# Kernel optimization log

Measured on AMD Instinct MI355X. Metric: run time of the kernel, lower is better.

Reference implementation:

```python
import jax, jax.numpy as jnp
import numpy as np

B, LQ, LK, H, NH = 2, 2048, 2048, 1024, 16
HD = H // NH


def setup_inputs() -> dict:
    key = jax.random.key(0)
    ks = jax.random.split(key, 7)
    s = 1.0 / np.sqrt(H)
    return {
        "decoder_hidden": jax.random.normal(ks[0], (B, LQ, H), jnp.float32),
        "encoder_hidden": jax.random.normal(ks[1], (B, LK, H), jnp.float32),
        "encoder_attention_mask": jnp.ones((B, LK), jnp.int32),
        "Wq": jax.random.normal(ks[2], (H, H), jnp.float32) * s,
        "Wk": jax.random.normal(ks[3], (H, H), jnp.float32) * s,
        "Wv": jax.random.normal(ks[4], (H, H), jnp.float32) * s,
        "Wo": jax.random.normal(ks[5], (H, H), jnp.float32) * s,
        "bo": jnp.zeros((H,), jnp.float32),
    }


def reference(decoder_hidden, encoder_hidden, encoder_attention_mask, Wq, Wk, Wv, Wo, bo):
    # nn.Linear(bias=False): y = x @ W.T
    Q = jnp.einsum('bqh,oh->bqo', decoder_hidden, Wq)
    K = jnp.einsum('bkh,oh->bko', encoder_hidden, Wk)
    V = jnp.einsum('bkh,oh->bko', encoder_hidden, Wv)
    # [B, NH, L, HD]
    Q = Q.reshape(B, LQ, NH, HD).transpose(0, 2, 1, 3)
    K = K.reshape(B, LK, NH, HD).transpose(0, 2, 1, 3)
    V = V.reshape(B, LK, NH, HD).transpose(0, 2, 1, 3)
    scale = jnp.float32(HD) ** -0.5
    scores = jnp.einsum('bhqd,bhkd->bhqk', Q, K) * scale
    mask = (encoder_attention_mask[:, None, None, :] != 0)  # [B,1,1,LK]
    scores = jnp.where(mask, scores, -jnp.inf)
    weights = jax.nn.softmax(scores, axis=-1)
    # dropout is identity in eval mode
    context = jnp.einsum('bhqk,bhkd->bhqd', weights, V)
    context = context.transpose(0, 2, 1, 3).reshape(B, LQ, H)
    output = jnp.einsum('bqh,oh->bqo', context, Wo) + bo
    return output, weights
```

## Files before the change

### kernel.cpp

```cpp
#include <hip/hip_runtime.h>
#include <hip/hip_bf16.h>
#include <stdint.h>

typedef __attribute__((ext_vector_type(8))) short short8;
typedef __attribute__((ext_vector_type(4))) short s16x4;
typedef __attribute__((ext_vector_type(4))) float f32x4;

#define MFMA16(a,b,c)    __builtin_amdgcn_mfma_f32_16x16x32_bf16(a,b,c,0,0,0)
#define MFMA16K16(a,b,c) __builtin_amdgcn_mfma_f32_16x16x16bf16_1k(a,b,c,0,0,0)

static __device__ inline void gload_lds16(const void* g, void* l) {
  __builtin_amdgcn_global_load_lds((const __attribute__((address_space(1))) uint32_t*)g,
                                   (__attribute__((address_space(3))) uint32_t*)l, 16, 0, 0);
}

__global__ __launch_bounds__(256) void cvt_all(
    const float* __restrict__ dh, const float* __restrict__ eh,
    const float* __restrict__ Wq, const float* __restrict__ Wk,
    const float* __restrict__ Wv, const float* __restrict__ Wo,
    __hip_bfloat16* __restrict__ dhb, __hip_bfloat16* __restrict__ ehb,
    __hip_bfloat16* __restrict__ wqb, __hip_bfloat16* __restrict__ wkb,
    __hip_bfloat16* __restrict__ wvb, __hip_bfloat16* __restrict__ wob)
{
  int idx = blockIdx.x * 256 + threadIdx.x;
  const float* src; __hip_bfloat16* dst; int off;
  if      (idx <  524288) { src=dh; dst=dhb; off=idx; }
  else if (idx < 1048576) { src=eh; dst=ehb; off=idx-524288; }
  else if (idx < 1179648) { src=Wq; dst=wqb; off=idx-1048576; }
  else if (idx < 1310720) { src=Wk; dst=wkb; off=idx-1179648; }
  else if (idx < 1441792) { src=Wv; dst=wvb; off=idx-1310720; }
  else                    { src=Wo; dst=wob; off=idx-1441792; }
  float4 a = ((const float4*)src)[off*2+0];
  float4 b = ((const float4*)src)[off*2+1];
  union { short8 v; __hip_bfloat16 h[8]; } u;
  u.h[0]=__float2bfloat16(a.x); u.h[1]=__float2bfloat16(a.y);
  u.h[2]=__float2bfloat16(a.z); u.h[3]=__float2bfloat16(a.w);
  u.h[4]=__float2bfloat16(b.x); u.h[5]=__float2bfloat16(b.y);
  u.h[6]=__float2bfloat16(b.z); u.h[7]=__float2bfloat16(b.w);
  ((short8*)dst)[off] = u.v;
}

__device__ inline void gemm_core(const __hip_bfloat16* __restrict__ A,
                                 const __hip_bfloat16* __restrict__ W,
                                 int bm, int bn, int K, f32x4 (&acc)[4][4]) {
  __shared__ __hip_bfloat16 sA[128*64];
  __shared__ __hip_bfloat16 sB[128*64];
  const int t = threadIdx.x, lane = t & 63, wvi = t >> 6, g = lane >> 4, i = lane & 15;
  const int wm = wvi >> 1, wn = wvi & 1;
  const f32x4 z4 = {0.f,0.f,0.f,0.f};
  for (int m=0;m<4;m++) for (int n=0;n<4;n++) acc[m][n]=z4;
  const int nkt = K >> 6;
  for (int kt=0; kt<nkt; ++kt) {
    for (int c=0;c<4;c++) {
      int idx = c*256+t, row = idx>>3, slot = idx&7;
      int sc = (slot ^ (row&7))*8;
      gload_lds16(A + (size_t)(bm*128+row)*K + kt*64 + sc, (char*)sA + c*4096 + wvi*1024);
    }
    for (int c=0;c<4;c++) {
      int idx = c*256+t, row = idx>>3, slot = idx&7;
      int sc = (slot ^ (row&7))*8;
      gload_lds16(W + (size_t)(bn*128+row)*K + kt*64 + sc, (char*)sB + c*4096 + wvi*1024);
    }
    __syncthreads();
    short8 af[4][2], bf[4][2];
    for (int m=0;m<4;m++) {
      int row = wm*64 + m*16 + i;
      af[m][0] = *(const short8*)&sA[row*64 + ((g     ^ (row&7)))*8];
      af[m][1] = *(const short8*)&sA[row*64 + (((4+g) ^ (row&7)))*8];
    }
    for (int n=0;n<4;n++) {
      int row = wn*64 + n*16 + i;
      bf[n][0] = *(const short8*)&sB[row*64 + ((g     ^ (row&7)))*8];
      bf[n][1] = *(const short8*)&sB[row*64 + (((4+g) ^ (row&7)))*8];
    }
    for (int m=0;m<4;m++) for (int n=0;n<4;n++) {
      acc[m][n] = MFMA16(af[m][0], bf[n][0], acc[m][n]);
      acc[m][n] = MFMA16(af[m][1], bf[n][1], acc[m][n]);
    }
    __syncthreads();
  }
}

__global__ __launch_bounds__(256) void gemm_qkv(
    const __hip_bfloat16* __restrict__ dhb, const __hip_bfloat16* __restrict__ ehb,
    const __hip_bfloat16* __restrict__ wqp, const __hip_bfloat16* __restrict__ wkp,
    const __hip_bfloat16* __restrict__ wvp,
    __hip_bfloat16* __restrict__ Qb, __hip_bfloat16* __restrict__ Kb,
    __hip_bfloat16* __restrict__ Vt) {
  const int zz = blockIdx.z;
  const __hip_bfloat16* A = (zz==0) ? dhb : ehb;
  const __hip_bfloat16* W = (zz==0) ? wqp : (zz==1 ? wkp : wvp);
  f32x4 acc[4][4];
  gemm_core(A, W, blockIdx.x, blockIdx.y, 1024, acc);
  const int t = threadIdx.x, lane=t&63, w_=t>>6, g=lane>>4, i=lane&15;
  const int wm=w_>>1, wn=w_&1;
  if (zz != 2) {
    __hip_bfloat16* C = (zz==0) ? Qb : Kb;
    for (int m=0;m<4;m++) for (int n=0;n<4;n++) for (int r=0;r<4;r++) {
      int row = blockIdx.x*128 + wm*64 + m*16 + 4*g + r;
      int col = blockIdx.y*128 + wn*64 + n*16 + i;
      C[(size_t)row*1024 + col] = __float2bfloat16(acc[m][n][r]);
    }
  } else {
    for (int m=0;m<4;m++) for (int n=0;n<4;n++) {
      int row0 = blockIdx.x*128 + wm*64 + m*16 + 4*g;
      int bb = row0 >> 11, kin = row0 & 2047;
      int o = blockIdx.y*128 + wn*64 + n*16 + i;
      int hh = o >> 6, dd = o & 63;
      union { s16x4 v; __hip_bfloat16 h4[4]; } u;
      for (int r=0;r<4;r++) u.h4[r] = __float2bfloat16(acc[m][n][r]);
      *(s16x4*)&Vt[((size_t)((bb*16+hh)*64+dd))*2048 + kin] = u.v;
    }
  }
}

__global__ __launch_bounds__(256) void gemm_out(
    const __hip_bfloat16* __restrict__ ctx, const __hip_bfloat16* __restrict__ wop,
    const float* __restrict__ bias, float* __restrict__ out) {
  f32x4 acc[4][4];
  gemm_core(ctx, wop, blockIdx.x, blockIdx.y, 1024, acc);
  const int t = threadIdx.x, lane=t&63, w_=t>>6, g=lane>>4, i=lane&15;
  const int wm=w_>>1, wn=w_&1;
  for (int m=0;m<4;m++) for (int n=0;n<4;n++) for (int r=0;r<4;r++) {
    int row = blockIdx.x*128 + wm*64 + m*16 + 4*g + r;
    int col = blockIdx.y*128 + wn*64 + n*16 + i;
    out[(size_t)row*1024 + col] = acc[m][n][r] + bias[col];
  }
}

__global__ __launch_bounds__(256, 4) void attn_kernel(
    const __hip_bfloat16* __restrict__ Qb, const __hip_bfloat16* __restrict__ Kb,
    const __hip_bfloat16* __restrict__ Vt, const int* __restrict__ mask,
    float* __restrict__ wout, __hip_bfloat16* __restrict__ ctx)
{
  __shared__ char smem[32768];
  const int t = threadIdx.x, lane = t&63, wv_ = t>>6, g = lane>>4, i = lane&15;
  const int qt = blockIdx.x, bh = blockIdx.y, b = bh>>4, h = bh&15;
  const int q0 = qt*64 + wv_*16;
  const float scale = 0.125f;
  const f32x4 z4 = {0.f,0.f,0.f,0.f};

  short8 qf[2];
  { const __hip_bfloat16* qrow = Qb + (size_t)(b*2048 + q0 + i)*1024 + h*64;
    qf[0] = *(const short8*)(qrow + g*8);
    qf[1] = *(const short8*)(qrow + 32 + g*8); }

  f32x4 acc[4];
  for (int z=0;z<4;z++) acc[z] = z4;
  float lsum = 0.0f;

  const int* mbase = mask + b*2048;

#define STAGE_KV(buf, kt_) do { \
    _Pragma("unroll") \
    for (int c=0;c<2;c++) { \
      int idx_ = c*256 + t; int row_ = idx_>>3, slot_ = idx_&7; \
      int sc_ = (slot_ ^ (row_&7)) * 8; \
      gload_lds16(Kb + (size_t)(b*2048 + (kt_)*64 + row_)*1024 + h*64 + sc_, \
                  smem + (buf)*8192 + c*4096 + wv_*1024); \
      gload_lds16(Vt + (size_t)((b*16+h)*64 + row_)*2048 + (kt_)*64 + sc_, \
                  smem + 16384 + (buf)*8192 + c*4096 + wv_*1024); \
    } } while(0)

#define STAGE_K(buf, kt_) do { \
    _Pragma("unroll") \
    for (int c=0;c<2;c++) { \
      int idx_ = c*256 + t; int row_ = idx_>>3, slot_ = idx_&7; \
      int sc_ = (slot_ ^ (row_&7)) * 8; \
      gload_lds16(Kb + (size_t)(b*2048 + (kt_)*64 + row_)*1024 + h*64 + sc_, \
                  smem + (buf)*8192 + c*4096 + wv_*1024); \
    } } while(0)

  int cur = 0;
  STAGE_KV(0, 0);
  __syncthreads();
  for (int kt=0; kt<32; ++kt) {
    if (kt+1 < 32) STAGE_KV(cur^1, kt+1);
    const __hip_bfloat16* sKc = (const __hip_bfloat16*)(smem + cur*8192);
    const __hip_bfloat16* sVc = (const __hip_bfloat16*)(smem + 16384 + cur*8192);
    #pragma unroll
    for (int cb=0; cb<4; ++cb) {
      int row = cb*16 + i;
      short8 kf0 = *(const short8*)&sKc[row*64 + ((g     ^ (row&7)))*8];
      short8 kf1 = *(const short8*)&sKc[row*64 + (((4+g) ^ (row&7)))*8];
      f32x4 st = MFMA16(kf0, qf[0], z4);
      st = MFMA16(kf1, qf[1], st);
      int4 m4 = *(const int4*)&mbase[kt*64 + cb*16 + 4*g];
      float p0 = m4.x ? __expf(st[0]*scale) : 0.0f;
      float p1 = m4.y ? __expf(st[1]*scale) : 0.0f;
      float p2 = m4.z ? __expf(st[2]*scale) : 0.0f;
      float p3 = m4.w ? __expf(st[3]*scale) : 0.0f;
      lsum += (p0+p1)+(p2+p3);
      union { s16x4 v; __hip_bfloat16 hh[4]; } pk;
      pk.hh[0] = __float2bfloat16(p0);
      pk.hh[1] = __float2bfloat16(p1);
      pk.hh[2] = __float2bfloat16(p2);
      pk.hh[3] = __float2bfloat16(p3);
      #pragma unroll
      for (int blk=0; blk<4; ++blk) {
        int vrow = blk*16 + i;
        const s16x4 vtf = *(const s16x4*)&sVc[vrow*64 +
            (((2*cb + (g>>1)) ^ (vrow&7)))*8 + 4*(g&1)];
        acc[blk] = MFMA16K16(pk.v, vtf, acc[blk]);
      }
    }
    __syncthreads();
    cur ^= 1;
  }

  lsum += __shfl_xor(lsum, 16);
  lsum += __shfl_xor(lsum, 32);
  const float linvq = 1.0f / lsum;

  float linvr[4];
  #pragma unroll
  for (int r=0;r<4;r++) linvr[r] = __shfl(linvq, (lane & 48) | (4*g + r));

  #pragma unroll
  for (int blk=0;blk<4;blk++)
    #pragma unroll
    for (int r=0;r<4;r++) {
      int q = q0 + 4*g + r;
      ctx[(size_t)(b*2048 + q)*1024 + h*64 + blk*16 + i] =
          __float2bfloat16(acc[blk][r]*linvr[r]);
    }

  STAGE_K(0, 0);
  __syncthreads();

  char* sT = smem + 16384 + wv_*4096;

  cur = 0;
  for (int kt=0; kt<32; ++kt) {
    if (kt+1 < 32) STAGE_K(cur^1, kt+1);
    asm volatile("" ::: "memory");
    const __hip_bfloat16* sKc = (const __hip_bfloat16*)(smem + cur*8192);
    #pragma unroll
    for (int cb=0; cb<4; ++cb) {
      int row = cb*16 + i;
      short8 kf0 = *(const short8*)&sKc[row*64 + ((g     ^ (row&7)))*8];
      short8 kf1 = *(const short8*)&sKc[row*64 + (((4+g) ^ (row&7)))*8];
      f32x4 st = MFMA16(kf0, qf[0], z4);
      st = MFMA16(kf1, qf[1], st);
      int4 m4 = *(const int4*)&mbase[kt*64 + cb*16 + 4*g];
      f32x4 w4;
      w4[0] = m4.x ? __expf(st[0]*scale)*linvq : 0.f;
      w4[1] = m4.y ? __expf(st[1]*scale)*linvq : 0.f;
      w4[2] = m4.z ? __expf(st[2]*scale)*linvq : 0.f;
      w4[3] = m4.w ? __expf(st[3]*scale)*linvq : 0.f;
      *(f32x4*)(sT + i*256 + (((cb*4 + g) ^ i) * 16)) = w4;
    }
    #pragma unroll
    for (int s=0; s<4; ++s) {
      int rho = 4*s + g;
      f32x4 w4 = *(const f32x4*)(sT + rho*256 + ((i ^ rho) * 16));
      __builtin_nontemporal_store(w4,
          (f32x4*)&wout[((size_t)bh*2048 + q0 + rho)*2048 + kt*64 + i*4]);
    }
    asm volatile("s_waitcnt vmcnt(4)" ::: "memory");
    __builtin_amdgcn_s_barrier();
    cur ^= 1;
  }
#undef STAGE_KV
#undef STAGE_K
}

extern "C" void kernel_launch(void* const* d_in, const int* in_sizes, int n_in,
                              void* d_out, int out_size, void* d_ws, size_t ws_size,
                              hipStream_t stream) {
  const float* dh  = (const float*)d_in[0];
  const float* eh  = (const float*)d_in[1];
  const int*  mask = (const int*)d_in[2];
  const float* Wq  = (const float*)d_in[3];
  const float* Wk  = (const float*)d_in[4];
  const float* Wv  = (const float*)d_in[5];
  const float* Wo  = (const float*)d_in[6];
  const float* bo  = (const float*)d_in[7];
  float* out  = (float*)d_out;
  float* wout = out + (size_t)2*2048*1024;

  char* ws = (char*)d_ws;
  __hip_bfloat16* dhb = (__hip_bfloat16*)(ws + 0);
  __hip_bfloat16* ehb = (__hip_bfloat16*)(ws + 8388608);
  __hip_bfloat16* wqb = (__hip_bfloat16*)(ws + 16777216);
  __hip_bfloat16* wkb = (__hip_bfloat16*)(ws + 18874368);
  __hip_bfloat16* wvb = (__hip_bfloat16*)(ws + 20971520);
  __hip_bfloat16* wob = (__hip_bfloat16*)(ws + 23068672);
  __hip_bfloat16* Qb  = (__hip_bfloat16*)(ws + 25165824);
  __hip_bfloat16* Kb  = (__hip_bfloat16*)(ws + 33554432);
  __hip_bfloat16* Vtb = (__hip_bfloat16*)(ws + 41943040);
  __hip_bfloat16* ctxb= (__hip_bfloat16*)(ws + 50331648);

  cvt_all<<<6144, 256, 0, stream>>>(dh, eh, Wq, Wk, Wv, Wo,
                                    dhb, ehb, wqb, wkb, wvb, wob);
  gemm_qkv<<<dim3(32, 8, 3), 256, 0, stream>>>(dhb, ehb, wqb, wkb, wvb, Qb, Kb, Vtb);
  attn_kernel<<<dim3(32, 32), 256, 0, stream>>>(Qb, Kb, Vtb, mask, wout, ctxb);
  gemm_out<<<dim3(32, 8), 256, 0, stream>>>(ctxb, wob, bo, out);
}
```

Before: 242.2 us.

## Split attention into row-sum pass and fused normalized-weights plus PV pass

The single attention kernel is split in two. A new lightweight kernel computes only the softmax denominators per query row and stores their inverses in workspace. A second kernel then makes one pass over K/V that writes the normalized weights and also accumulates P·V from the already-normalized bf16 probabilities. Before, QK^T and exp were recomputed over two full loops in one kernel, with the second loop loading only K. The change trades that for an extra launch, a second kernel that loads K again, and higher LDS use (48KB, occupancy bound 3). Context now accumulates normalized bf16 weights, which slightly changes rounding.

```diff
diff --git a/kernel.cpp b/kernel.cpp
--- a/kernel.cpp
+++ b/kernel.cpp
@@ -128,12 +128,11 @@
   }
 }
 
-__global__ __launch_bounds__(256, 4) void attn_kernel(
+__global__ __launch_bounds__(256, 4) void attn_lsum(
     const __hip_bfloat16* __restrict__ Qb, const __hip_bfloat16* __restrict__ Kb,
-    const __hip_bfloat16* __restrict__ Vt, const int* __restrict__ mask,
-    float* __restrict__ wout, __hip_bfloat16* __restrict__ ctx)
+    const int* __restrict__ mask, float* __restrict__ linv_buf)
 {
-  __shared__ char smem[32768];
+  __shared__ char smem[16384];
   const int t = threadIdx.x, lane = t&63, wv_ = t>>6, g = lane>>4, i = lane&15;
   const int qt = blockIdx.x, bh = blockIdx.y, b = bh>>4, h = bh&15;
   const int q0 = qt*64 + wv_*16;
@@ -145,11 +144,72 @@
     qf[0] = *(const short8*)(qrow + g*8);
     qf[1] = *(const short8*)(qrow + 32 + g*8); }
 
+  const int* mbase = mask + b*2048;
+  float lsum = 0.0f;
+
+#define STAGE_K_L(buf, kt_) do { \
+    _Pragma("unroll") \
+    for (int c=0;c<2;c++) { \
+      int idx_ = c*256 + t; int row_ = idx_>>3, slot_ = idx_&7; \
+      int sc_ = (slot_ ^ (row_&7)) * 8; \
+      gload_lds16(Kb + (size_t)(b*2048 + (kt_)*64 + row_)*1024 + h*64 + sc_, \
+                  smem + (buf)*8192 + c*4096 + wv_*1024); \
+    } } while(0)
+
+  int cur = 0;
+  STAGE_K_L(0, 0);
+  __syncthreads();
+  for (int kt=0; kt<32; ++kt) {
+    if (kt+1 < 32) STAGE_K_L(cur^1, kt+1);
+    const __hip_bfloat16* sKc = (const __hip_bfloat16*)(smem + cur*8192);
+    #pragma unroll
+    for (int cb=0; cb<4; ++cb) {
+      int row = cb*16 + i;
+      short8 kf0 = *(const short8*)&sKc[row*64 + ((g     ^ (row&7)))*8];
+      short8 kf1 = *(const short8*)&sKc[row*64 + (((4+g) ^ (row&7)))*8];
+      f32x4 st = MFMA16(kf0, qf[0], z4);
+      st = MFMA16(kf1, qf[1], st);
+      int4 m4 = *(const int4*)&mbase[kt*64 + cb*16 + 4*g];
+      lsum += (m4.x ? __expf(st[0]*scale) : 0.0f) + (m4.y ? __expf(st[1]*scale) : 0.0f)
+            + (m4.z ? __expf(st[2]*scale) : 0.0f) + (m4.w ? __expf(st[3]*scale) : 0.0f);
+    }
+    __syncthreads();
+    cur ^= 1;
+  }
+#undef STAGE_K_L
+
+  lsum += __shfl_xor(lsum, 16);
+  lsum += __shfl_xor(lsum, 32);
+  if (lane < 16)
+    linv_buf[(size_t)bh*2048 + q0 + i] = 1.0f / lsum;
+}
+
+__global__ __launch_bounds__(256, 3) void attn_main(
+    const __hip_bfloat16* __restrict__ Qb, const __hip_bfloat16* __restrict__ Kb,
+    const __hip_bfloat16* __restrict__ Vt, const int* __restrict__ mask,
+    const float* __restrict__ linv_buf,
+    float* __restrict__ wout, __hip_bfloat16* __restrict__ ctx)
+{
+  __shared__ char smem[49152];
+  const int t = threadIdx.x, lane = t&63, wv_ = t>>6, g = lane>>4, i = lane&15;
+  const int qt = blockIdx.x, bh = blockIdx.y, b = bh>>4, h = bh&15;
+  const int q0 = qt*64 + wv_*16;
+  const float scale = 0.125f;
+  const f32x4 z4 = {0.f,0.f,0.f,0.f};
+
+  short8 qf[2];
+  { const __hip_bfloat16* qrow = Qb + (size_t)(b*2048 + q0 + i)*1024 + h*64;
+    qf[0] = *(const short8*)(qrow + g*8);
+    qf[1] = *(const short8*)(qrow + 32 + g*8); }
+
+  const float linvq = linv_buf[(size_t)bh*2048 + q0 + i];
+
   f32x4 acc[4];
   for (int z=0;z<4;z++) acc[z] = z4;
-  float lsum = 0.0f;
 
   const int* mbase = mask + b*2048;
+  char* sT = smem + 32768 + wv_*4096;
+  float* wrow_base = wout + ((size_t)bh*2048 + q0)*2048;
 
 #define STAGE_KV(buf, kt_) do { \
     _Pragma("unroll") \
@@ -162,79 +222,16 @@
                   smem + 16384 + (buf)*8192 + c*4096 + wv_*1024); \
     } } while(0)
 
-#define STAGE_K(buf, kt_) do { \
-    _Pragma("unroll") \
-    for (int c=0;c<2;c++) { \
-      int idx_ = c*256 + t; int row_ = idx_>>3, slot_ = idx_&7; \
-      int sc_ = (slot_ ^ (row_&7)) * 8; \
-      gload_lds16(Kb + (size_t)(b*2048 + (kt_)*64 + row_)*1024 + h*64 + sc_, \
-                  smem + (buf)*8192 + c*4096 + wv_*1024); \
-    } } while(0)
-
   int cur = 0;
   STAGE_KV(0, 0);
   __syncthreads();
   for (int kt=0; kt<32; ++kt) {
     if (kt+1 < 32) STAGE_KV(cur^1, kt+1);
+    asm volatile("" ::: "memory");
     const __hip_bfloat16* sKc = (const __hip_bfloat16*)(smem + cur*8192);
     const __hip_bfloat16* sVc = (const __hip_bfloat16*)(smem + 16384 + cur*8192);
-    #pragma unroll
-    for (int cb=0; cb<4; ++cb) {
-      int row = cb*16 + i;
-      short8 kf0 = *(const short8*)&sKc[row*64 + ((g     ^ (row&7)))*8];
-      short8 kf1 = *(const short8*)&sKc[row*64 + (((4+g) ^ (row&7)))*8];
-      f32x4 st = MFMA16(kf0, qf[0], z4);
-      st = MFMA16(kf1, qf[1], st);
-      int4 m4 = *(const int4*)&mbase[kt*64 + cb*16 + 4*g];
-      float p0 = m4.x ? __expf(st[0]*scale) : 0.0f;
-      float p1 = m4.y ? __expf(st[1]*scale) : 0.0f;
-      float p2 = m4.z ? __expf(st[2]*scale) : 0.0f;
-      float p3 = m4.w ? __expf(st[3]*scale) : 0.0f;
-      lsum += (p0+p1)+(p2+p3);
-      union { s16x4 v; __hip_bfloat16 hh[4]; } pk;
-      pk.hh[0] = __float2bfloat16(p0);
-      pk.hh[1] = __float2bfloat16(p1);
-      pk.hh[2] = __float2bfloat16(p2);
-      pk.hh[3] = __float2bfloat16(p3);
-      #pragma unroll
-      for (int blk=0; blk<4; ++blk) {
-        int vrow = blk*16 + i;
-        const s16x4 vtf = *(const s16x4*)&sVc[vrow*64 +
-            (((2*cb + (g>>1)) ^ (vrow&7)))*8 + 4*(g&1)];
-        acc[blk] = MFMA16K16(pk.v, vtf, acc[blk]);
-      }
-    }
-    __syncthreads();
-    cur ^= 1;
-  }
-
-  lsum += __shfl_xor(lsum, 16);
-  lsum += __shfl_xor(lsum, 32);
-  const float linvq = 1.0f / lsum;
-
-  float linvr[4];
-  #pragma unroll
-  for (int r=0;r<4;r++) linvr[r] = __shfl(linvq, (lane & 48) | (4*g + r));
-
-  #pragma unroll
-  for (int blk=0;blk<4;blk++)
-    #pragma unroll
-    for (int r=0;r<4;r++) {
-      int q = q0 + 4*g + r;
-      ctx[(size_t)(b*2048 + q)*1024 + h*64 + blk*16 + i] =
-          __float2bfloat16(acc[blk][r]*linvr[r]);
-    }
-
-  STAGE_K(0, 0);
-  __syncthreads();
-
-  char* sT = smem + 16384 + wv_*4096;
-
-  cur = 0;
-  for (int kt=0; kt<32; ++kt) {
-    if (kt+1 < 32) STAGE_K(cur^1, kt+1);
-    asm volatile("" ::: "memory");
-    const __hip_bfloat16* sKc = (const __hip_bfloat16*)(smem + cur*8192);
+
+    s16x4 pk[4];
     #pragma unroll
     for (int cb=0; cb<4; ++cb) {
       int row = cb*16 + i;
@@ -249,20 +246,45 @@
       w4[2] = m4.z ? __expf(st[2]*scale)*linvq : 0.f;
       w4[3] = m4.w ? __expf(st[3]*scale)*linvq : 0.f;
       *(f32x4*)(sT + i*256 + (((cb*4 + g) ^ i) * 16)) = w4;
-    }
+      union { s16x4 v; __hip_bfloat16 hh[4]; } u;
+      u.hh[0]=__float2bfloat16(w4[0]); u.hh[1]=__float2bfloat16(w4[1]);
+      u.hh[2]=__float2bfloat16(w4[2]); u.hh[3]=__float2bfloat16(w4[3]);
+      pk[cb] = u.v;
+    }
+
     #pragma unroll
     for (int s=0; s<4; ++s) {
       int rho = 4*s + g;
       f32x4 w4 = *(const f32x4*)(sT + rho*256 + ((i ^ rho) * 16));
       __builtin_nontemporal_store(w4,
-          (f32x4*)&wout[((size_t)bh*2048 + q0 + rho)*2048 + kt*64 + i*4]);
-    }
+          (f32x4*)&wrow_base[(size_t)rho*2048 + kt*64 + i*4]);
+    }
+
+    #pragma unroll
+    for (int cb=0; cb<4; ++cb) {
+      #pragma unroll
+      for (int blk=0; blk<4; ++blk) {
+        int vrow = blk*16 + i;
+        const s16x4 vtf = *(const s16x4*)&sVc[vrow*64 +
+            (((2*cb + (g>>1)) ^ (vrow&7)))*8 + 4*(g&1)];
+        acc[blk] = MFMA16K16(pk[cb], vtf, acc[blk]);
+      }
+    }
+
     asm volatile("s_waitcnt vmcnt(4)" ::: "memory");
     __builtin_amdgcn_s_barrier();
     cur ^= 1;
   }
 #undef STAGE_KV
-#undef STAGE_K
+
+  #pragma unroll
+  for (int blk=0;blk<4;blk++)
+    #pragma unroll
+    for (int r=0;r<4;r++) {
+      int q = q0 + 4*g + r;
+      ctx[(size_t)(b*2048 + q)*1024 + h*64 + blk*16 + i] =
+          __float2bfloat16(acc[blk][r]);
+    }
 }
 
 extern "C" void kernel_launch(void* const* d_in, const int* in_sizes, int n_in,
@@ -290,10 +312,12 @@
   __hip_bfloat16* Kb  = (__hip_bfloat16*)(ws + 33554432);
   __hip_bfloat16* Vtb = (__hip_bfloat16*)(ws + 41943040);
   __hip_bfloat16* ctxb= (__hip_bfloat16*)(ws + 50331648);
+  float* linvb        = (float*)(ws + 58720256);
 
   cvt_all<<<6144, 256, 0, stream>>>(dh, eh, Wq, Wk, Wv, Wo,
                                     dhb, ehb, wqb, wkb, wvb, wob);
   gemm_qkv<<<dim3(32, 8, 3), 256, 0, stream>>>(dhb, ehb, wqb, wkb, wvb, Qb, Kb, Vtb);
-  attn_kernel<<<dim3(32, 32), 256, 0, stream>>>(Qb, Kb, Vtb, mask, wout, ctxb);
+  attn_lsum<<<dim3(32, 32), 256, 0, stream>>>(Qb, Kb, mask, linvb);
+  attn_main<<<dim3(32, 32), 256, 0, stream>>>(Qb, Kb, Vtb, mask, linvb, wout, ctxb);
   gemm_out<<<dim3(32, 8), 256, 0, stream>>>(ctxb, wob, bo, out);
 }
```

After: 272.3 us. 1.12x slower.

## Pair two query tiles per block and overlap weight writes with second tile's PV pass

Applied to the files above, without the earlier changes.

Each block now processes two 64-row query tiles. The weight-writing pass for tile A runs inside the same K/V loop as tile B's softmax-sum and PV accumulation, so one K/V sweep is shared between them. The aim is to replace one of the four full K sweeps per pair of tiles and to overlap the large weight stores with MFMA work. In exchange the kernel uses more registers and LDS (48KB, launch bound 2), and the grid is halved to 512 blocks, which lowers occupancy and parallelism.

```diff
diff --git a/kernel.cpp b/kernel.cpp
--- a/kernel.cpp
+++ b/kernel.cpp
@@ -128,28 +128,29 @@
   }
 }
 
-__global__ __launch_bounds__(256, 4) void attn_kernel(
+__global__ __launch_bounds__(256, 2) void attn_pair(
     const __hip_bfloat16* __restrict__ Qb, const __hip_bfloat16* __restrict__ Kb,
     const __hip_bfloat16* __restrict__ Vt, const int* __restrict__ mask,
     float* __restrict__ wout, __hip_bfloat16* __restrict__ ctx)
 {
-  __shared__ char smem[32768];
+  __shared__ char smem[49152];
   const int t = threadIdx.x, lane = t&63, wv_ = t>>6, g = lane>>4, i = lane&15;
-  const int qt = blockIdx.x, bh = blockIdx.y, b = bh>>4, h = bh&15;
-  const int q0 = qt*64 + wv_*16;
+  const int bh = blockIdx.y, b = bh>>4, h = bh&15;
+  const int q0A = blockIdx.x*128 + wv_*16;
+  const int q0B = q0A + 64;
   const float scale = 0.125f;
   const f32x4 z4 = {0.f,0.f,0.f,0.f};
 
-  short8 qf[2];
-  { const __hip_bfloat16* qrow = Qb + (size_t)(b*2048 + q0 + i)*1024 + h*64;
-    qf[0] = *(const short8*)(qrow + g*8);
-    qf[1] = *(const short8*)(qrow + 32 + g*8); }
-
-  f32x4 acc[4];
-  for (int z=0;z<4;z++) acc[z] = z4;
-  float lsum = 0.0f;
+  short8 qfA[2], qfB[2];
+  { const __hip_bfloat16* qr = Qb + (size_t)(b*2048 + q0A + i)*1024 + h*64;
+    qfA[0] = *(const short8*)(qr + g*8);
+    qfA[1] = *(const short8*)(qr + 32 + g*8);
+    const __hip_bfloat16* qr2 = Qb + (size_t)(b*2048 + q0B + i)*1024 + h*64;
+    qfB[0] = *(const short8*)(qr2 + g*8);
+    qfB[1] = *(const short8*)(qr2 + 32 + g*8); }
 
   const int* mbase = mask + b*2048;
+  char* sT = smem + 32768 + wv_*4096;
 
 #define STAGE_KV(buf, kt_) do { \
     _Pragma("unroll") \
@@ -171,6 +172,9 @@
                   smem + (buf)*8192 + c*4096 + wv_*1024); \
     } } while(0)
 
+  f32x4 acc[4];
+  for (int z=0;z<4;z++) acc[z] = z4;
+  float lsum = 0.0f;
   int cur = 0;
   STAGE_KV(0, 0);
   __syncthreads();
@@ -183,8 +187,8 @@
       int row = cb*16 + i;
       short8 kf0 = *(const short8*)&sKc[row*64 + ((g     ^ (row&7)))*8];
       short8 kf1 = *(const short8*)&sKc[row*64 + (((4+g) ^ (row&7)))*8];
-      f32x4 st = MFMA16(kf0, qf[0], z4);
-      st = MFMA16(kf1, qf[1], st);
+      f32x4 st = MFMA16(kf0, qfA[0], z4);
+      st = MFMA16(kf1, qfA[1], st);
       int4 m4 = *(const int4*)&mbase[kt*64 + cb*16 + 4*g];
       float p0 = m4.x ? __expf(st[0]*scale) : 0.0f;
       float p1 = m4.y ? __expf(st[1]*scale) : 0.0f;
@@ -192,10 +196,8 @@
       float p3 = m4.w ? __expf(st[3]*scale) : 0.0f;
       lsum += (p0+p1)+(p2+p3);
       union { s16x4 v; __hip_bfloat16 hh[4]; } pk;
-      pk.hh[0] = __float2bfloat16(p0);
-      pk.hh[1] = __float2bfloat16(p1);
-      pk.hh[2] = __float2bfloat16(p2);
-      pk.hh[3] = __float2bfloat16(p3);
+      pk.hh[0]=__float2bfloat16(p0); pk.hh[1]=__float2bfloat16(p1);
+      pk.hh[2]=__float2bfloat16(p2); pk.hh[3]=__float2bfloat16(p3);
       #pragma unroll
       for (int blk=0; blk<4; ++blk) {
         int vrow = blk*16 + i;
@@ -207,30 +209,99 @@
     __syncthreads();
     cur ^= 1;
   }
-
   lsum += __shfl_xor(lsum, 16);
   lsum += __shfl_xor(lsum, 32);
-  const float linvq = 1.0f / lsum;
-
-  float linvr[4];
-  #pragma unroll
-  for (int r=0;r<4;r++) linvr[r] = __shfl(linvq, (lane & 48) | (4*g + r));
-
-  #pragma unroll
-  for (int blk=0;blk<4;blk++)
-    #pragma unroll
-    for (int r=0;r<4;r++) {
-      int q = q0 + 4*g + r;
-      ctx[(size_t)(b*2048 + q)*1024 + h*64 + blk*16 + i] =
-          __float2bfloat16(acc[blk][r]*linvr[r]);
-    }
-
+  const float linvA = 1.0f / lsum;
+  { float linvr[4];
+    #pragma unroll
+    for (int r=0;r<4;r++) linvr[r] = __shfl(linvA, (lane & 48) | (4*g + r));
+    #pragma unroll
+    for (int blk=0;blk<4;blk++)
+      #pragma unroll
+      for (int r=0;r<4;r++) {
+        int q = q0A + 4*g + r;
+        ctx[(size_t)(b*2048 + q)*1024 + h*64 + blk*16 + i] =
+            __float2bfloat16(acc[blk][r]*linvr[r]);
+      } }
+
+  for (int z=0;z<4;z++) acc[z] = z4;
+  lsum = 0.0f;
+  float* wrowA = wout + ((size_t)bh*2048 + q0A)*2048;
+  cur = 0;
+  STAGE_KV(0, 0);
+  __syncthreads();
+  for (int kt=0; kt<32; ++kt) {
+    if (kt+1 < 32) STAGE_KV(cur^1, kt+1);
+    asm volatile("" ::: "memory");
+    const __hip_bfloat16* sKc = (const __hip_bfloat16*)(smem + cur*8192);
+    const __hip_bfloat16* sVc = (const __hip_bfloat16*)(smem + 16384 + cur*8192);
+    s16x4 pkB[4];
+    #pragma unroll
+    for (int cb=0; cb<4; ++cb) {
+      int row = cb*16 + i;
+      short8 kf0 = *(const short8*)&sKc[row*64 + ((g     ^ (row&7)))*8];
+      short8 kf1 = *(const short8*)&sKc[row*64 + (((4+g) ^ (row&7)))*8];
+      int4 m4 = *(const int4*)&mbase[kt*64 + cb*16 + 4*g];
+      f32x4 stA = MFMA16(kf0, qfA[0], z4);
+      stA = MFMA16(kf1, qfA[1], stA);
+      f32x4 w4;
+      w4[0] = m4.x ? __expf(stA[0]*scale)*linvA : 0.f;
+      w4[1] = m4.y ? __expf(stA[1]*scale)*linvA : 0.f;
+      w4[2] = m4.z ? __expf(stA[2]*scale)*linvA : 0.f;
+      w4[3] = m4.w ? __expf(stA[3]*scale)*linvA : 0.f;
+      *(f32x4*)(sT + i*256 + (((cb*4 + g) ^ i) * 16)) = w4;
+      f32x4 stB = MFMA16(kf0, qfB[0], z4);
+      stB = MFMA16(kf1, qfB[1], stB);
+      float p0 = m4.x ? __expf(stB[0]*scale) : 0.0f;
+      float p1 = m4.y ? __expf(stB[1]*scale) : 0.0f;
+      float p2 = m4.z ? __expf(stB[2]*scale) : 0.0f;
+      float p3 = m4.w ? __expf(stB[3]*scale) : 0.0f;
+      lsum += (p0+p1)+(p2+p3);
+      union { s16x4 v; __hip_bfloat16 hh[4]; } pk;
+      pk.hh[0]=__float2bfloat16(p0); pk.hh[1]=__float2bfloat16(p1);
+      pk.hh[2]=__float2bfloat16(p2); pk.hh[3]=__float2bfloat16(p3);
+      pkB[cb] = pk.v;
+    }
+    #pragma unroll
+    for (int s=0; s<4; ++s) {
+      int rho = 4*s + g;
+      f32x4 w4 = *(const f32x4*)(sT + rho*256 + ((i ^ rho) * 16));
+      __builtin_nontemporal_store(w4,
+          (f32x4*)&wrowA[(size_t)rho*2048 + kt*64 + i*4]);
+    }
+    #pragma unroll
+    for (int cb=0; cb<4; ++cb) {
+      #pragma unroll
+      for (int blk=0; blk<4; ++blk) {
+        int vrow = blk*16 + i;
+        const s16x4 vtf = *(const s16x4*)&sVc[vrow*64 +
+            (((2*cb + (g>>1)) ^ (vrow&7)))*8 + 4*(g&1)];
+        acc[blk] = MFMA16K16(pkB[cb], vtf, acc[blk]);
+      }
+    }
+    asm volatile("s_waitcnt vmcnt(4)" ::: "memory");
+    __builtin_amdgcn_s_barrier();
+    cur ^= 1;
+  }
+  lsum += __shfl_xor(lsum, 16);
+  lsum += __shfl_xor(lsum, 32);
+  const float linvB = 1.0f / lsum;
+  { float linvr[4];
+    #pragma unroll
+    for (int r=0;r<4;r++) linvr[r] = __shfl(linvB, (lane & 48) | (4*g + r));
+    #pragma unroll
+    for (int blk=0;blk<4;blk++)
+      #pragma unroll
+      for (int r=0;r<4;r++) {
+        int q = q0B + 4*g + r;
+        ctx[(size_t)(b*2048 + q)*1024 + h*64 + blk*16 + i] =
+            __float2bfloat16(acc[blk][r]*linvr[r]);
+      } }
+
+  float* wrowB = wout + ((size_t)bh*2048 + q0B)*2048;
+  cur = 0;
   STAGE_K(0, 0);
   __syncthreads();
-
-  char* sT = smem + 16384 + wv_*4096;
-
-  cur = 0;
   for (int kt=0; kt<32; ++kt) {
     if (kt+1 < 32) STAGE_K(cur^1, kt+1);
     asm volatile("" ::: "memory");
@@ -240,14 +311,14 @@
       int row = cb*16 + i;
       short8 kf0 = *(const short8*)&sKc[row*64 + ((g     ^ (row&7)))*8];
       short8 kf1 = *(const short8*)&sKc[row*64 + (((4+g) ^ (row&7)))*8];
-      f32x4 st = MFMA16(kf0, qf[0], z4);
-      st = MFMA16(kf1, qf[1], st);
+      f32x4 st = MFMA16(kf0, qfB[0], z4);
+      st = MFMA16(kf1, qfB[1], st);
       int4 m4 = *(const int4*)&mbase[kt*64 + cb*16 + 4*g];
       f32x4 w4;
-      w4[0] = m4.x ? __expf(st[0]*scale)*linvq : 0.f;
-      w4[1] = m4.y ? __expf(st[1]*scale)*linvq : 0.f;
-      w4[2] = m4.z ? __expf(st[2]*scale)*linvq : 0.f;
-      w4[3] = m4.w ? __expf(st[3]*scale)*linvq : 0.f;
+      w4[0] = m4.x ? __expf(st[0]*scale)*linvB : 0.f;
+      w4[1] = m4.y ? __expf(st[1]*scale)*linvB : 0.f;
+      w4[2] = m4.z ? __expf(st[2]*scale)*linvB : 0.f;
+      w4[3] = m4.w ? __expf(st[3]*scale)*linvB : 0.f;
       *(f32x4*)(sT + i*256 + (((cb*4 + g) ^ i) * 16)) = w4;
     }
     #pragma unroll
@@ -255,7 +326,7 @@
       int rho = 4*s + g;
       f32x4 w4 = *(const f32x4*)(sT + rho*256 + ((i ^ rho) * 16));
       __builtin_nontemporal_store(w4,
-          (f32x4*)&wout[((size_t)bh*2048 + q0 + rho)*2048 + kt*64 + i*4]);
+          (f32x4*)&wrowB[(size_t)rho*2048 + kt*64 + i*4]);
     }
     asm volatile("s_waitcnt vmcnt(4)" ::: "memory");
     __builtin_amdgcn_s_barrier();
@@ -294,6 +365,6 @@
   cvt_all<<<6144, 256, 0, stream>>>(dh, eh, Wq, Wk, Wv, Wo,
                                     dhb, ehb, wqb, wkb, wvb, wob);
   gemm_qkv<<<dim3(32, 8, 3), 256, 0, stream>>>(dhb, ehb, wqb, wkb, wvb, Qb, Kb, Vtb);
-  attn_kernel<<<dim3(32, 32), 256, 0, stream>>>(Qb, Kb, Vtb, mask, wout, ctxb);
+  attn_pair<<<dim3(16, 32), 256, 0, stream>>>(Qb, Kb, Vtb, mask, wout, ctxb);
   gemm_out<<<dim3(32, 8), 256, 0, stream>>>(ctxb, wob, bo, out);
 }
```

Result: faster. 231.5 us, median of 2 (-4.4%).

## Process two query tiles per wave to reuse staged K/V across 128 rows

Applied to the files above, without the earlier changes.

Each attention block now handles 128 query rows instead of 64. Every wave keeps two 16-row Q fragments and reuses each K/V fragment read from LDS for both, which halves K/V global staging and LDS reads per query. The grid shrinks to 16x32 blocks, and launch bounds drop to 2 blocks per SM with a larger shared buffer. This raises register pressure and lowers occupancy, and fewer blocks (512) may leave some compute units underused.

```diff
diff --git a/kernel.cpp b/kernel.cpp
--- a/kernel.cpp
+++ b/kernel.cpp
@@ -128,28 +128,29 @@
   }
 }
 
-__global__ __launch_bounds__(256, 4) void attn_kernel(
+__global__ __launch_bounds__(256, 2) void attn_gh(
     const __hip_bfloat16* __restrict__ Qb, const __hip_bfloat16* __restrict__ Kb,
     const __hip_bfloat16* __restrict__ Vt, const int* __restrict__ mask,
     float* __restrict__ wout, __hip_bfloat16* __restrict__ ctx)
 {
-  __shared__ char smem[32768];
+  __shared__ char smem[49152];
   const int t = threadIdx.x, lane = t&63, wv_ = t>>6, g = lane>>4, i = lane&15;
-  const int qt = blockIdx.x, bh = blockIdx.y, b = bh>>4, h = bh&15;
-  const int q0 = qt*64 + wv_*16;
+  const int bh = blockIdx.y, b = bh>>4, h = bh&15;
+  const int q0A = blockIdx.x*128 + wv_*16;
+  const int q0B = q0A + 64;
   const float scale = 0.125f;
   const f32x4 z4 = {0.f,0.f,0.f,0.f};
 
-  short8 qf[2];
-  { const __hip_bfloat16* qrow = Qb + (size_t)(b*2048 + q0 + i)*1024 + h*64;
-    qf[0] = *(const short8*)(qrow + g*8);
-    qf[1] = *(const short8*)(qrow + 32 + g*8); }
-
-  f32x4 acc[4];
-  for (int z=0;z<4;z++) acc[z] = z4;
-  float lsum = 0.0f;
+  short8 qfA[2], qfB[2];
+  { const __hip_bfloat16* qr = Qb + (size_t)(b*2048 + q0A + i)*1024 + h*64;
+    qfA[0] = *(const short8*)(qr + g*8);
+    qfA[1] = *(const short8*)(qr + 32 + g*8);
+    const __hip_bfloat16* qr2 = Qb + (size_t)(b*2048 + q0B + i)*1024 + h*64;
+    qfB[0] = *(const short8*)(qr2 + g*8);
+    qfB[1] = *(const short8*)(qr2 + 32 + g*8); }
 
   const int* mbase = mask + b*2048;
+  char* sT = smem + 32768 + wv_*4096;
 
 #define STAGE_KV(buf, kt_) do { \
     _Pragma("unroll") \
@@ -171,6 +172,10 @@
                   smem + (buf)*8192 + c*4096 + wv_*1024); \
     } } while(0)
 
+  f32x4 accA[4], accB[4];
+  #pragma unroll
+  for (int z=0;z<4;z++) { accA[z]=z4; accB[z]=z4; }
+  float lsumA = 0.0f, lsumB = 0.0f;
   int cur = 0;
   STAGE_KV(0, 0);
   __syncthreads();
@@ -178,86 +183,124 @@
     if (kt+1 < 32) STAGE_KV(cur^1, kt+1);
     const __hip_bfloat16* sKc = (const __hip_bfloat16*)(smem + cur*8192);
     const __hip_bfloat16* sVc = (const __hip_bfloat16*)(smem + 16384 + cur*8192);
+    s16x4 pkA[4], pkB[4];
     #pragma unroll
     for (int cb=0; cb<4; ++cb) {
       int row = cb*16 + i;
       short8 kf0 = *(const short8*)&sKc[row*64 + ((g     ^ (row&7)))*8];
       short8 kf1 = *(const short8*)&sKc[row*64 + (((4+g) ^ (row&7)))*8];
-      f32x4 st = MFMA16(kf0, qf[0], z4);
-      st = MFMA16(kf1, qf[1], st);
       int4 m4 = *(const int4*)&mbase[kt*64 + cb*16 + 4*g];
-      float p0 = m4.x ? __expf(st[0]*scale) : 0.0f;
-      float p1 = m4.y ? __expf(st[1]*scale) : 0.0f;
-      float p2 = m4.z ? __expf(st[2]*scale) : 0.0f;
-      float p3 = m4.w ? __expf(st[3]*scale) : 0.0f;
-      lsum += (p0+p1)+(p2+p3);
-      union { s16x4 v; __hip_bfloat16 hh[4]; } pk;
-      pk.hh[0] = __float2bfloat16(p0);
-      pk.hh[1] = __float2bfloat16(p1);
-      pk.hh[2] = __float2bfloat16(p2);
-      pk.hh[3] = __float2bfloat16(p3);
+      f32x4 stA = MFMA16(kf0, qfA[0], z4);
+      stA = MFMA16(kf1, qfA[1], stA);
+      f32x4 stB = MFMA16(kf0, qfB[0], z4);
+      stB = MFMA16(kf1, qfB[1], stB);
+      float a0 = m4.x ? __expf(stA[0]*scale) : 0.0f;
+      float a1 = m4.y ? __expf(stA[1]*scale) : 0.0f;
+      float a2 = m4.z ? __expf(stA[2]*scale) : 0.0f;
+      float a3 = m4.w ? __expf(stA[3]*scale) : 0.0f;
+      lsumA += (a0+a1)+(a2+a3);
+      float b0 = m4.x ? __expf(stB[0]*scale) : 0.0f;
+      float b1 = m4.y ? __expf(stB[1]*scale) : 0.0f;
+      float b2 = m4.z ? __expf(stB[2]*scale) : 0.0f;
+      float b3 = m4.w ? __expf(stB[3]*scale) : 0.0f;
+      lsumB += (b0+b1)+(b2+b3);
+      union { s16x4 v; __hip_bfloat16 hh[4]; } ua, ub;
+      ua.hh[0]=__float2bfloat16(a0); ua.hh[1]=__float2bfloat16(a1);
+      ua.hh[2]=__float2bfloat16(a2); ua.hh[3]=__float2bfloat16(a3);
+      ub.hh[0]=__float2bfloat16(b0); ub.hh[1]=__float2bfloat16(b1);
+      ub.hh[2]=__float2bfloat16(b2); ub.hh[3]=__float2bfloat16(b3);
+      pkA[cb] = ua.v; pkB[cb] = ub.v;
+    }
+    #pragma unroll
+    for (int cb=0; cb<4; ++cb) {
       #pragma unroll
       for (int blk=0; blk<4; ++blk) {
         int vrow = blk*16 + i;
         const s16x4 vtf = *(const s16x4*)&sVc[vrow*64 +
             (((2*cb + (g>>1)) ^ (vrow&7)))*8 + 4*(g&1)];
-        acc[blk] = MFMA16K16(pk.v, vtf, acc[blk]);
+        accA[blk] = MFMA16K16(pkA[cb], vtf, accA[blk]);
+        accB[blk] = MFMA16K16(pkB[cb], vtf, accB[blk]);
       }
     }
     __syncthreads();
     cur ^= 1;
   }
 
-  lsum += __shfl_xor(lsum, 16);
-  lsum += __shfl_xor(lsum, 32);
-  const float linvq = 1.0f / lsum;
-
-  float linvr[4];
-  #pragma unroll
-  for (int r=0;r<4;r++) linvr[r] = __shfl(linvq, (lane & 48) | (4*g + r));
-
-  #pragma unroll
-  for (int blk=0;blk<4;blk++)
+  lsumA += __shfl_xor(lsumA, 16);
+  lsumA += __shfl_xor(lsumA, 32);
+  lsumB += __shfl_xor(lsumB, 16);
+  lsumB += __shfl_xor(lsumB, 32);
+  const float linvA = 1.0f / lsumA;
+  const float linvB = 1.0f / lsumB;
+  { float lrA[4], lrB[4];
     #pragma unroll
     for (int r=0;r<4;r++) {
-      int q = q0 + 4*g + r;
-      ctx[(size_t)(b*2048 + q)*1024 + h*64 + blk*16 + i] =
-          __float2bfloat16(acc[blk][r]*linvr[r]);
-    }
-
+      lrA[r] = __shfl(linvA, (lane & 48) | (4*g + r));
+      lrB[r] = __shfl(linvB, (lane & 48) | (4*g + r));
+    }
+    #pragma unroll
+    for (int blk=0;blk<4;blk++)
+      #pragma unroll
+      for (int r=0;r<4;r++) {
+        int qa = q0A + 4*g + r;
+        ctx[(size_t)(b*2048 + qa)*1024 + h*64 + blk*16 + i] =
+            __float2bfloat16(accA[blk][r]*lrA[r]);
+        int qb = q0B + 4*g + r;
+        ctx[(size_t)(b*2048 + qb)*1024 + h*64 + blk*16 + i] =
+            __float2bfloat16(accB[blk][r]*lrB[r]);
+      } }
+
+  float* wrowA = wout + ((size_t)bh*2048 + q0A)*2048;
+  float* wrowB = wout + ((size_t)bh*2048 + q0B)*2048;
+  cur = 0;
   STAGE_K(0, 0);
   __syncthreads();
-
-  char* sT = smem + 16384 + wv_*4096;
-
-  cur = 0;
   for (int kt=0; kt<32; ++kt) {
     if (kt+1 < 32) STAGE_K(cur^1, kt+1);
     asm volatile("" ::: "memory");
     const __hip_bfloat16* sKc = (const __hip_bfloat16*)(smem + cur*8192);
+    f32x4 w4B[4];
     #pragma unroll
     for (int cb=0; cb<4; ++cb) {
       int row = cb*16 + i;
       short8 kf0 = *(const short8*)&sKc[row*64 + ((g     ^ (row&7)))*8];
       short8 kf1 = *(const short8*)&sKc[row*64 + (((4+g) ^ (row&7)))*8];
-      f32x4 st = MFMA16(kf0, qf[0], z4);
-      st = MFMA16(kf1, qf[1], st);
       int4 m4 = *(const int4*)&mbase[kt*64 + cb*16 + 4*g];
-      f32x4 w4;
-      w4[0] = m4.x ? __expf(st[0]*scale)*linvq : 0.f;
-      w4[1] = m4.y ? __expf(st[1]*scale)*linvq : 0.f;
-      w4[2] = m4.z ? __expf(st[2]*scale)*linvq : 0.f;
-      w4[3] = m4.w ? __expf(st[3]*scale)*linvq : 0.f;
-      *(f32x4*)(sT + i*256 + (((cb*4 + g) ^ i) * 16)) = w4;
+      f32x4 stA = MFMA16(kf0, qfA[0], z4);
+      stA = MFMA16(kf1, qfA[1], stA);
+      f32x4 wa;
+      wa[0] = m4.x ? __expf(stA[0]*scale)*linvA : 0.f;
+      wa[1] = m4.y ? __expf(stA[1]*scale)*linvA : 0.f;
+      wa[2] = m4.z ? __expf(stA[2]*scale)*linvA : 0.f;
+      wa[3] = m4.w ? __expf(stA[3]*scale)*linvA : 0.f;
+      *(f32x4*)(sT + i*256 + (((cb*4 + g) ^ i) * 16)) = wa;
+      f32x4 stB = MFMA16(kf0, qfB[0], z4);
+      stB = MFMA16(kf1, qfB[1], stB);
+      f32x4 wb;
+      wb[0] = m4.x ? __expf(stB[0]*scale)*linvB : 0.f;
+      wb[1] = m4.y ? __expf(stB[1]*scale)*linvB : 0.f;
+      wb[2] = m4.z ? __expf(stB[2]*scale)*linvB : 0.f;
+      wb[3] = m4.w ? __expf(stB[3]*scale)*linvB : 0.f;
+      w4B[cb] = wb;
     }
     #pragma unroll
     for (int s=0; s<4; ++s) {
       int rho = 4*s + g;
       f32x4 w4 = *(const f32x4*)(sT + rho*256 + ((i ^ rho) * 16));
       __builtin_nontemporal_store(w4,
-          (f32x4*)&wout[((size_t)bh*2048 + q0 + rho)*2048 + kt*64 + i*4]);
-    }
-    asm volatile("s_waitcnt vmcnt(4)" ::: "memory");
+          (f32x4*)&wrowA[(size_t)rho*2048 + kt*64 + i*4]);
+    }
+    #pragma unroll
+    for (int cb=0; cb<4; ++cb)
+      *(f32x4*)(sT + i*256 + (((cb*4 + g) ^ i) * 16)) = w4B[cb];
+    #pragma unroll
+    for (int s=0; s<4; ++s) {
+      int rho = 4*s + g;
+      f32x4 w4 = *(const f32x4*)(sT + rho*256 + ((i ^ rho) * 16));
+      __builtin_nontemporal_store(w4,
+          (f32x4*)&wrowB[(size_t)rho*2048 + kt*64 + i*4]);
+    }
+    asm volatile("s_waitcnt vmcnt(8)" ::: "memory");
     __builtin_amdgcn_s_barrier();
     cur ^= 1;
   }
@@ -294,6 +337,6 @@
   cvt_all<<<6144, 256, 0, stream>>>(dh, eh, Wq, Wk, Wv, Wo,
                                     dhb, ehb, wqb, wkb, wvb, wob);
   gemm_qkv<<<dim3(32, 8, 3), 256, 0, stream>>>(dhb, ehb, wqb, wkb, wvb, Qb, Kb, Vtb);
-  attn_kernel<<<dim3(32, 32), 256, 0, stream>>>(Qb, Kb, Vtb, mask, wout, ctxb);
+  attn_gh<<<dim3(16, 32), 256, 0, stream>>>(Qb, Kb, Vtb, mask, wout, ctxb);
   gemm_out<<<dim3(32, 8), 256, 0, stream>>>(ctxb, wob, bo, out);
 }
```

New measurement: 269.8 us. 11.4% more time.
